# Performance work log

Hardware: AMD Instinct MI355X
Metric: run time of the kernel (lower is better)

The kernel has to match this reference:

```python
import jax, jax.numpy as jnp
import numpy as np

MAX_DEG = 6


def neighbor_lookup(atoms, edges, maskvalue, include_self):
    # atoms: (B, A, F), edges: (B, A, D) with -1 padding
    B, A, F = atoms.shape
    D = edges.shape[-1]
    mask = edges >= 0
    idx = jnp.where(mask, edges, 0).reshape(B, A * D)
    g = jnp.take_along_axis(atoms, idx[:, :, None], axis=1).reshape(B, A, D, F)
    g = jnp.where(mask[..., None], g, maskvalue)
    if include_self:
        g = jnp.concatenate([atoms[:, :, None, :], g], axis=2)  # (B,A,D+1,F)
    return g


def graph_conv(atoms, bonds, edges, W, b):
    # W: (MAX_DEG, F_in+BF, C), b: (MAX_DEG, C)
    deg = (edges >= 0).sum(-1)  # (B, A)
    summed_atoms = neighbor_lookup(atoms, edges, 0.0, True).sum(2)  # self + neighbors
    summed_bonds = bonds.sum(2)
    feats = jnp.concatenate([summed_atoms, summed_bonds], axis=-1)
    out = jnp.zeros(feats.shape[:2] + (W.shape[-1],), feats.dtype)
    for d in range(MAX_DEG):  # small fixed loop over degrees
        h = jax.nn.relu(feats @ W[d] + b[d])
        out = out + jnp.where((deg == d)[..., None], h, 0.0)
    return out


def graph_pool(atoms, edges):
    g = neighbor_lookup(atoms, edges, -jnp.inf, True)  # self included -> finite max
    return g.max(axis=2)


def graph_output(atoms, bonds, edges, Wo, bo):
    deg = (edges >= 0).sum(-1)
    feats = jnp.concatenate([atoms, bonds.sum(2)], axis=-1)
    out = jax.nn.softmax(feats @ Wo + bo, axis=-1)
    mask = (deg != 0)[..., None]  # zero out padded atoms
    return jnp.where(mask, out, 0.0).sum(axis=1)  # (B, hid)


def setup_inputs():
    key = jax.random.key(0)
    ks = jax.random.split(key, 16)
    B, A, D = 4096, 64, 6
    AF, BF, H = 37, 6, 128
    s = lambda k, sh: (jax.random.normal(k, sh, jnp.float32) * 0.05)
    return {
        "atoms": jax.random.normal(ks[0], (B, A, AF), jnp.float32),
        "bonds": jax.random.normal(ks[1], (B, A, D, BF), jnp.float32),
        "edges": jax.random.randint(ks[2], (B, A, D), -1, A),
        "W1": s(ks[3], (MAX_DEG, AF + BF, H)),
        "b1": s(ks[4], (MAX_DEG, H)),
        "W2": s(ks[5], (MAX_DEG, H + BF, H)),
        "b2": s(ks[6], (MAX_DEG, H)),
        "Wo": s(ks[7], (H + BF, H)),
        "bo": s(ks[8], (H,)),
        "Wm1": s(ks[9], (H, H // 2)),
        "bm1": s(ks[10], (H // 2,)),
        "Wm2": s(ks[11], (H // 2, H // 4)),
        "bm2": s(ks[12], (H // 4,)),
        "Wm3": s(ks[13], (H // 4, 1)),
        "bm3": s(ks[14], (1,)),
    }


def reference(atoms, bonds, edges, W1, b1, W2, b2, Wo, bo, Wm1, bm1, Wm2, bm2, Wm3, bm3):
    x = graph_conv(atoms, bonds, edges, W1, b1)
    x = graph_pool(x, edges)
    x = graph_conv(x, bonds, edges, W2, b2)
    x = graph_pool(x, edges)
    fp = graph_output(x, bonds, edges, Wo, bo)
    h = jax.nn.relu(fp @ Wm1 + bm1)
    h = jax.nn.relu(h @ Wm2 + bm2)
    out = (h @ Wm3 + bm3).squeeze()  # (B,)
    return out
```

## Files before the change

### kernel.cpp

```cpp
#include <hip/hip_runtime.h>
#include <math.h>


__device__ __forceinline__ float4 max4(float4 a, float4 b) {
  return make_float4(fmaxf(a.x, b.x), fmaxf(a.y, b.y), fmaxf(a.z, b.z), fmaxf(a.w, b.w));
}

__device__ __forceinline__ float4 nbr_max(const float4* sx4, const int* se, int a, int c4) {
  float4 m = sx4[a * 32 + c4];
#pragma unroll
  for (int d = 0; d < 6; ++d) {
    int e = se[a * 6 + d];
    if (e >= 0) m = max4(m, sx4[e * 32 + c4]);
  }
  return m;
}

__device__ __forceinline__ float4 nbr_sum(const float4* sx4, const int* se, int a, int c4) {
  float4 s = sx4[a * 32 + c4];
#pragma unroll
  for (int d = 0; d < 6; ++d) {
    int e = se[a * 6 + d];
    if (e >= 0) {
      float4 v = sx4[e * 32 + c4];
      s.x += v.x; s.y += v.y; s.z += v.z; s.w += v.w;
    }
  }
  return s;
}

__device__ __forceinline__ float4 nbr_wmax(const float4* sx4, const int* se, const int* sdeg,
                                           int a, int c4) {
  float4 m = make_float4(0.f, 0.f, 0.f, 0.f);
  if (sdeg[a] < 6) m = max4(m, sx4[a * 32 + c4]);
#pragma unroll
  for (int d = 0; d < 6; ++d) {
    int e = se[a * 6 + d];
    if (e >= 0 && sdeg[e] < 6) m = max4(m, sx4[e * 32 + c4]);
  }
  return m;
}

__global__ __launch_bounds__(256, 4) void qsar_fused(
    const float* __restrict__ atoms, const float* __restrict__ bonds,
    const int* __restrict__ edges,
    const float* __restrict__ W1, const float* __restrict__ b1,
    const float* __restrict__ W2, const float* __restrict__ b2,
    const float* __restrict__ Wo, const float* __restrict__ bo,
    const float* __restrict__ Wm1, const float* __restrict__ bm1,
    const float* __restrict__ Wm2, const float* __restrict__ bm2,
    const float* __restrict__ Wm3, const float* __restrict__ bm3,
    float* __restrict__ out)
{
  const int b    = blockIdx.x;
  const int tid  = threadIdx.x;
  const int wid  = tid >> 6;
  const int hid  = tid >> 5;
  const int hl   = tid & 31;

  __shared__ float s_x[64 * 128];
  __shared__ float s_sa[16 * 38];
  __shared__ float s_bsum[64 * 8];
  __shared__ int   s_edges[64 * 6];
  __shared__ int   s_deg[64];
  __shared__ int   s_work[64];
  __shared__ int   s_perm[64];
  __shared__ float s_rsum[64];
  __shared__ int   s_nwork, s_na, s_nz;

  float4* sx4  = reinterpret_cast<float4*>(s_x);
  float*  s_fp = s_sa;
  float*  s_h1 = s_sa + 256;
  float*  s_h2 = s_sa + 320;

  {
    const int* ge = edges + (size_t)b * (64 * 6);
    for (int i = tid; i < 64 * 6; i += 256) s_edges[i] = ge[i];
    const float* gb = bonds + (size_t)b * (64 * 36);
    for (int i = tid; i < 64 * 6; i += 256) {
      int a = i / 6, f = i - a * 6;
      float s = 0.f;
#pragma unroll
      for (int d = 0; d < 6; ++d) s += gb[a * 36 + d * 6 + f];
      s_bsum[a * 8 + f] = s;
    }
#pragma unroll
    for (int j = 0; j < 8; ++j) sx4[tid + j * 256] = make_float4(0.f, 0.f, 0.f, 0.f);
    if (tid == 0) { s_nwork = 0; s_na = 0; s_nz = 0; }
  }
  __syncthreads();

  if (tid < 64) {
    int dcnt = 0;
#pragma unroll
    for (int d = 0; d < 6; ++d) dcnt += (s_edges[tid * 6 + d] >= 0) ? 1 : 0;
    s_deg[tid] = dcnt;
    if (dcnt < 6) { int p = atomicAdd(&s_nwork, 1); s_work[p] = tid; }
  }
  __syncthreads();

  if (tid < 64) {
    int nzf = (s_deg[tid] < 6) ? 1 : 0;
#pragma unroll
    for (int d = 0; d < 6; ++d) {
      int e = s_edges[tid * 6 + d];
      if (e >= 0 && s_deg[e] < 6) nzf = 1;
    }
    if (nzf) { int p = atomicAdd(&s_na, 1); s_perm[p] = tid; }
    else     { int p = atomicAdd(&s_nz, 1); s_perm[63 - p] = tid; }
  }

  {
    const int nw = s_nwork;
    const float* ga = atoms + (size_t)b * (64 * 37);
    const int c0 = hl * 4;
    for (int cb = 0; cb < nw; cb += 16) {
      const int cnt = (nw - cb < 16) ? (nw - cb) : 16;
      for (int i = tid; i < cnt * 37; i += 256) {
        int wi = i / 37, k = i - wi * 37;
        int a = s_work[cb + wi];
        float f = ga[a * 37 + k];
#pragma unroll
        for (int d = 0; d < 6; ++d) {
          int e = s_edges[a * 6 + d];
          if (e >= 0) f += ga[e * 37 + k];
        }
        s_sa[wi * 38 + k] = f;
      }
      __syncthreads();
      for (int w = hid; w < cnt; w += 8) {
        const int a = s_work[cb + w];
        const int d = s_deg[a];
        const float* wp = W1 + d * (43 * 128);
        float4 acc = *reinterpret_cast<const float4*>(&b1[d * 128 + c0]);
#pragma unroll 4
        for (int k = 0; k < 37; ++k) {
          const float f = s_sa[w * 38 + k];
          const float4 w4 = *reinterpret_cast<const float4*>(&wp[k * 128 + c0]);
          acc.x = fmaf(f, w4.x, acc.x); acc.y = fmaf(f, w4.y, acc.y);
          acc.z = fmaf(f, w4.z, acc.z); acc.w = fmaf(f, w4.w, acc.w);
        }
#pragma unroll
        for (int kk = 0; kk < 6; ++kk) {
          const float f = s_bsum[a * 8 + kk];
          const float4 w4 = *reinterpret_cast<const float4*>(&wp[(37 + kk) * 128 + c0]);
          acc.x = fmaf(f, w4.x, acc.x); acc.y = fmaf(f, w4.y, acc.y);
          acc.z = fmaf(f, w4.z, acc.z); acc.w = fmaf(f, w4.w, acc.w);
        }
        *reinterpret_cast<float4*>(&s_x[a * 128 + c0]) =
            make_float4(fmaxf(acc.x, 0.f), fmaxf(acc.y, 0.f),
                        fmaxf(acc.z, 0.f), fmaxf(acc.w, 0.f));
      }
      __syncthreads();
    }
  }
  __syncthreads();

  {
    float4 v0 = nbr_max(sx4, s_edges, (tid + 0 * 256) >> 5, tid & 31);
    float4 v1 = nbr_max(sx4, s_edges, (tid + 1 * 256) >> 5, tid & 31);
    float4 v2 = nbr_max(sx4, s_edges, (tid + 2 * 256) >> 5, tid & 31);
    float4 v3 = nbr_max(sx4, s_edges, (tid + 3 * 256) >> 5, tid & 31);
    float4 v4 = nbr_max(sx4, s_edges, (tid + 4 * 256) >> 5, tid & 31);
    float4 v5 = nbr_max(sx4, s_edges, (tid + 5 * 256) >> 5, tid & 31);
    float4 v6 = nbr_max(sx4, s_edges, (tid + 6 * 256) >> 5, tid & 31);
    float4 v7 = nbr_max(sx4, s_edges, (tid + 7 * 256) >> 5, tid & 31);
    __syncthreads();
    sx4[tid + 0 * 256] = v0; sx4[tid + 1 * 256] = v1;
    sx4[tid + 2 * 256] = v2; sx4[tid + 3 * 256] = v3;
    sx4[tid + 4 * 256] = v4; sx4[tid + 5 * 256] = v5;
    sx4[tid + 6 * 256] = v6; sx4[tid + 7 * 256] = v7;
  }
  __syncthreads();

  {
    const float4 z = make_float4(0.f, 0.f, 0.f, 0.f);
    float4 v0 = z, v1 = z, v2 = z, v3 = z, v4 = z, v5 = z, v6 = z, v7 = z;
    if (s_deg[(tid + 0 * 256) >> 5] < 6) v0 = nbr_sum(sx4, s_edges, (tid + 0 * 256) >> 5, tid & 31);
    if (s_deg[(tid + 1 * 256) >> 5] < 6) v1 = nbr_sum(sx4, s_edges, (tid + 1 * 256) >> 5, tid & 31);
    if (s_deg[(tid + 2 * 256) >> 5] < 6) v2 = nbr_sum(sx4, s_edges, (tid + 2 * 256) >> 5, tid & 31);
    if (s_deg[(tid + 3 * 256) >> 5] < 6) v3 = nbr_sum(sx4, s_edges, (tid + 3 * 256) >> 5, tid & 31);
    if (s_deg[(tid + 4 * 256) >> 5] < 6) v4 = nbr_sum(sx4, s_edges, (tid + 4 * 256) >> 5, tid & 31);
    if (s_deg[(tid + 5 * 256) >> 5] < 6) v5 = nbr_sum(sx4, s_edges, (tid + 5 * 256) >> 5, tid & 31);
    if (s_deg[(tid + 6 * 256) >> 5] < 6) v6 = nbr_sum(sx4, s_edges, (tid + 6 * 256) >> 5, tid & 31);
    if (s_deg[(tid + 7 * 256) >> 5] < 6) v7 = nbr_sum(sx4, s_edges, (tid + 7 * 256) >> 5, tid & 31);
    __syncthreads();
    if (s_deg[(tid + 0 * 256) >> 5] < 6) sx4[tid + 0 * 256] = v0;
    if (s_deg[(tid + 1 * 256) >> 5] < 6) sx4[tid + 1 * 256] = v1;
    if (s_deg[(tid + 2 * 256) >> 5] < 6) sx4[tid + 2 * 256] = v2;
    if (s_deg[(tid + 3 * 256) >> 5] < 6) sx4[tid + 3 * 256] = v3;
    if (s_deg[(tid + 4 * 256) >> 5] < 6) sx4[tid + 4 * 256] = v4;
    if (s_deg[(tid + 5 * 256) >> 5] < 6) sx4[tid + 5 * 256] = v5;
    if (s_deg[(tid + 6 * 256) >> 5] < 6) sx4[tid + 6 * 256] = v6;
    if (s_deg[(tid + 7 * 256) >> 5] < 6) sx4[tid + 7 * 256] = v7;
  }
  __syncthreads();

  {
    const int nw = s_nwork;
    const int c0 = hl * 4;
    for (int w = hid; w < nw; w += 8) {
      const int a = s_work[w];
      const int d = s_deg[a];
      const float* wp = W2 + d * (134 * 128);
      float4 acc = *reinterpret_cast<const float4*>(&b2[d * 128 + c0]);
#pragma unroll 4
      for (int k = 0; k < 128; ++k) {
        const float f = s_x[a * 128 + k];
        const float4 w4 = *reinterpret_cast<const float4*>(&wp[k * 128 + c0]);
        acc.x = fmaf(f, w4.x, acc.x); acc.y = fmaf(f, w4.y, acc.y);
        acc.z = fmaf(f, w4.z, acc.z); acc.w = fmaf(f, w4.w, acc.w);
      }
#pragma unroll
      for (int kk = 0; kk < 6; ++kk) {
        const float f = s_bsum[a * 8 + kk];
        const float4 w4 = *reinterpret_cast<const float4*>(&wp[(128 + kk) * 128 + c0]);
        acc.x = fmaf(f, w4.x, acc.x); acc.y = fmaf(f, w4.y, acc.y);
        acc.z = fmaf(f, w4.z, acc.z); acc.w = fmaf(f, w4.w, acc.w);
      }
      *reinterpret_cast<float4*>(&s_x[a * 128 + c0]) =
          make_float4(fmaxf(acc.x, 0.f), fmaxf(acc.y, 0.f),
                      fmaxf(acc.z, 0.f), fmaxf(acc.w, 0.f));
    }
  }
  __syncthreads();

  {
    float4 v0 = nbr_wmax(sx4, s_edges, s_deg, (tid + 0 * 256) >> 5, tid & 31);
    float4 v1 = nbr_wmax(sx4, s_edges, s_deg, (tid + 1 * 256) >> 5, tid & 31);
    float4 v2 = nbr_wmax(sx4, s_edges, s_deg, (tid + 2 * 256) >> 5, tid & 31);
    float4 v3 = nbr_wmax(sx4, s_edges, s_deg, (tid + 3 * 256) >> 5, tid & 31);
    float4 v4 = nbr_wmax(sx4, s_edges, s_deg, (tid + 4 * 256) >> 5, tid & 31);
    float4 v5 = nbr_wmax(sx4, s_edges, s_deg, (tid + 5 * 256) >> 5, tid & 31);
    float4 v6 = nbr_wmax(sx4, s_edges, s_deg, (tid + 6 * 256) >> 5, tid & 31);
    float4 v7 = nbr_wmax(sx4, s_edges, s_deg, (tid + 7 * 256) >> 5, tid & 31);
    __syncthreads();
    sx4[tid + 0 * 256] = v0; sx4[tid + 1 * 256] = v1;
    sx4[tid + 2 * 256] = v2; sx4[tid + 3 * 256] = v3;
    sx4[tid + 4 * 256] = v4; sx4[tid + 5 * 256] = v5;
    sx4[tid + 6 * 256] = v6; sx4[tid + 7 * 256] = v7;
  }
  __syncthreads();

  {
    const int cg = tid & 31, ag = hid;
    const int c0 = cg * 4;
    const int na = s_na;
    const int nr = (na + 31) >> 5;
    for (int j = 0; j < nr; ++j) {
      const int sl = j * 32 + ag * 4;
      const int at0 = s_perm[sl + 0], at1 = s_perm[sl + 1];
      const int at2 = s_perm[sl + 2], at3 = s_perm[sl + 3];
      float a00 = 0.f, a01 = 0.f, a02 = 0.f, a03 = 0.f;
      float a10 = 0.f, a11 = 0.f, a12 = 0.f, a13 = 0.f;
      float a20 = 0.f, a21 = 0.f, a22 = 0.f, a23 = 0.f;
      float a30 = 0.f, a31 = 0.f, a32 = 0.f, a33 = 0.f;
      if (j * 32 + wid * 8 < na) {
#pragma unroll 4
        for (int k = 0; k < 128; ++k) {
          const float4 w4 = *reinterpret_cast<const float4*>(Wo + k * 128 + c0);
          const float f0 = s_x[at0 * 128 + k], f1 = s_x[at1 * 128 + k];
          const float f2 = s_x[at2 * 128 + k], f3 = s_x[at3 * 128 + k];
          a00 = fmaf(f0, w4.x, a00); a01 = fmaf(f0, w4.y, a01);
          a02 = fmaf(f0, w4.z, a02); a03 = fmaf(f0, w4.w, a03);
          a10 = fmaf(f1, w4.x, a10); a11 = fmaf(f1, w4.y, a11);
          a12 = fmaf(f1, w4.z, a12); a13 = fmaf(f1, w4.w, a13);
          a20 = fmaf(f2, w4.x, a20); a21 = fmaf(f2, w4.y, a21);
          a22 = fmaf(f2, w4.z, a22); a23 = fmaf(f2, w4.w, a23);
          a30 = fmaf(f3, w4.x, a30); a31 = fmaf(f3, w4.y, a31);
          a32 = fmaf(f3, w4.z, a32); a33 = fmaf(f3, w4.w, a33);
        }
#pragma unroll
        for (int kk = 0; kk < 6; ++kk) {
          const float4 w4 = *reinterpret_cast<const float4*>(Wo + (128 + kk) * 128 + c0);
          const float f0 = s_bsum[at0 * 8 + kk], f1 = s_bsum[at1 * 8 + kk];
          const float f2 = s_bsum[at2 * 8 + kk], f3 = s_bsum[at3 * 8 + kk];
          a00 = fmaf(f0, w4.x, a00); a01 = fmaf(f0, w4.y, a01);
          a02 = fmaf(f0, w4.z, a02); a03 = fmaf(f0, w4.w, a03);
          a10 = fmaf(f1, w4.x, a10); a11 = fmaf(f1, w4.y, a11);
          a12 = fmaf(f1, w4.z, a12); a13 = fmaf(f1, w4.w, a13);
          a20 = fmaf(f2, w4.x, a20); a21 = fmaf(f2, w4.y, a21);
          a22 = fmaf(f2, w4.z, a22); a23 = fmaf(f2, w4.w, a23);
          a30 = fmaf(f3, w4.x, a30); a31 = fmaf(f3, w4.y, a31);
          a32 = fmaf(f3, w4.z, a32); a33 = fmaf(f3, w4.w, a33);
        }
      }
      __syncthreads();
      const float4 bo4 = *reinterpret_cast<const float4*>(bo + c0);
      if (sl + 0 < na)
        *reinterpret_cast<float4*>(&s_x[at0 * 128 + c0]) =
            make_float4(a00 + bo4.x, a01 + bo4.y, a02 + bo4.z, a03 + bo4.w);
      if (sl + 1 < na)
        *reinterpret_cast<float4*>(&s_x[at1 * 128 + c0]) =
            make_float4(a10 + bo4.x, a11 + bo4.y, a12 + bo4.z, a13 + bo4.w);
      if (sl + 2 < na)
        *reinterpret_cast<float4*>(&s_x[at2 * 128 + c0]) =
            make_float4(a20 + bo4.x, a21 + bo4.y, a22 + bo4.z, a23 + bo4.w);
      if (sl + 3 < na)
        *reinterpret_cast<float4*>(&s_x[at3 * 128 + c0]) =
            make_float4(a30 + bo4.x, a31 + bo4.y, a32 + bo4.z, a33 + bo4.w);
    }
    const int nz = 64 - na;
    for (int e = tid; e < nz * 128; e += 256) {
      int zi = e >> 7, c = e & 127;
      int a = s_perm[na + zi];
      float acc = bo[c];
#pragma unroll
      for (int kk = 0; kk < 6; ++kk)
        acc = fmaf(s_bsum[a * 8 + kk], Wo[(128 + kk) * 128 + c], acc);
      s_x[a * 128 + c] = acc;
    }
  }
  __syncthreads();

  {
    const int a = tid >> 2, q = tid & 3;
    float* base = &s_x[a * 128 + q * 32];
    const float4 v0 = *reinterpret_cast<const float4*>(base + ((0 + tid) & 7) * 4);
    const float4 v1 = *reinterpret_cast<const float4*>(base + ((1 + tid) & 7) * 4);
    const float4 v2 = *reinterpret_cast<const float4*>(base + ((2 + tid) & 7) * 4);
    const float4 v3 = *reinterpret_cast<const float4*>(base + ((3 + tid) & 7) * 4);
    const float4 v4 = *reinterpret_cast<const float4*>(base + ((4 + tid) & 7) * 4);
    const float4 v5 = *reinterpret_cast<const float4*>(base + ((5 + tid) & 7) * 4);
    const float4 v6 = *reinterpret_cast<const float4*>(base + ((6 + tid) & 7) * 4);
    const float4 v7 = *reinterpret_cast<const float4*>(base + ((7 + tid) & 7) * 4);
    float mx = fmaxf(fmaxf(fmaxf(v0.x, v0.y), fmaxf(v0.z, v0.w)),
                     fmaxf(fmaxf(v1.x, v1.y), fmaxf(v1.z, v1.w)));
    mx = fmaxf(mx, fmaxf(fmaxf(fmaxf(v2.x, v2.y), fmaxf(v2.z, v2.w)),
                         fmaxf(fmaxf(v3.x, v3.y), fmaxf(v3.z, v3.w))));
    mx = fmaxf(mx, fmaxf(fmaxf(fmaxf(v4.x, v4.y), fmaxf(v4.z, v4.w)),
                         fmaxf(fmaxf(v5.x, v5.y), fmaxf(v5.z, v5.w))));
    mx = fmaxf(mx, fmaxf(fmaxf(fmaxf(v6.x, v6.y), fmaxf(v6.z, v6.w)),
                         fmaxf(fmaxf(v7.x, v7.y), fmaxf(v7.z, v7.w))));
    mx = fmaxf(mx, __shfl_xor(mx, 1));
    mx = fmaxf(mx, __shfl_xor(mx, 2));
    float sm = 0.f;
    float4 e0, e1, e2, e3, e4, e5, e6, e7;
    e0.x = __expf(v0.x - mx); e0.y = __expf(v0.y - mx); e0.z = __expf(v0.z - mx); e0.w = __expf(v0.w - mx);
    e1.x = __expf(v1.x - mx); e1.y = __expf(v1.y - mx); e1.z = __expf(v1.z - mx); e1.w = __expf(v1.w - mx);
    e2.x = __expf(v2.x - mx); e2.y = __expf(v2.y - mx); e2.z = __expf(v2.z - mx); e2.w = __expf(v2.w - mx);
    e3.x = __expf(v3.x - mx); e3.y = __expf(v3.y - mx); e3.z = __expf(v3.z - mx); e3.w = __expf(v3.w - mx);
    e4.x = __expf(v4.x - mx); e4.y = __expf(v4.y - mx); e4.z = __expf(v4.z - mx); e4.w = __expf(v4.w - mx);
    e5.x = __expf(v5.x - mx); e5.y = __expf(v5.y - mx); e5.z = __expf(v5.z - mx); e5.w = __expf(v5.w - mx);
    e6.x = __expf(v6.x - mx); e6.y = __expf(v6.y - mx); e6.z = __expf(v6.z - mx); e6.w = __expf(v6.w - mx);
    e7.x = __expf(v7.x - mx); e7.y = __expf(v7.y - mx); e7.z = __expf(v7.z - mx); e7.w = __expf(v7.w - mx);
    sm += e0.x + e0.y + e0.z + e0.w; sm += e1.x + e1.y + e1.z + e1.w;
    sm += e2.x + e2.y + e2.z + e2.w; sm += e3.x + e3.y + e3.z + e3.w;
    sm += e4.x + e4.y + e4.z + e4.w; sm += e5.x + e5.y + e5.z + e5.w;
    sm += e6.x + e6.y + e6.z + e6.w; sm += e7.x + e7.y + e7.z + e7.w;
    *reinterpret_cast<float4*>(base + ((0 + tid) & 7) * 4) = e0;
    *reinterpret_cast<float4*>(base + ((1 + tid) & 7) * 4) = e1;
    *reinterpret_cast<float4*>(base + ((2 + tid) & 7) * 4) = e2;
    *reinterpret_cast<float4*>(base + ((3 + tid) & 7) * 4) = e3;
    *reinterpret_cast<float4*>(base + ((4 + tid) & 7) * 4) = e4;
    *reinterpret_cast<float4*>(base + ((5 + tid) & 7) * 4) = e5;
    *reinterpret_cast<float4*>(base + ((6 + tid) & 7) * 4) = e6;
    *reinterpret_cast<float4*>(base + ((7 + tid) & 7) * 4) = e7;
    sm += __shfl_xor(sm, 1);
    sm += __shfl_xor(sm, 2);
    if (q == 0) s_rsum[a] = (s_deg[a] != 0) ? (1.f / sm) : 0.f;
  }
  __syncthreads();

  {
    const int c = tid & 127, half = tid >> 7;
    float s = 0.f;
    for (int a2 = half * 32; a2 < half * 32 + 32; ++a2)
      s = fmaf(s_x[a2 * 128 + c], s_rsum[a2], s);
    s_fp[half * 128 + c] = s;
  }
  __syncthreads();
  if (tid < 128) s_fp[tid] += s_fp[128 + tid];
  __syncthreads();

  if (tid < 64) {
    float acc = bm1[tid];
    for (int k = 0; k < 128; ++k) acc = fmaf(s_fp[k], Wm1[k * 64 + tid], acc);
    s_h1[tid] = fmaxf(acc, 0.f);
  }
  __syncthreads();
  if (tid < 32) {
    float acc = bm2[tid];
    for (int k = 0; k < 64; ++k) acc = fmaf(s_h1[k], Wm2[k * 32 + tid], acc);
    s_h2[tid] = fmaxf(acc, 0.f);
  }
  __syncthreads();
  if (tid < 64) {
    float p = (tid < 32) ? s_h2[tid] * Wm3[tid] : 0.f;
#pragma unroll
    for (int off = 32; off > 0; off >>= 1) p += __shfl_xor(p, off);
    if (tid == 0) out[b] = p + bm3[0];
  }
}

extern "C" void kernel_launch(void* const* d_in, const int* in_sizes, int n_in,
                              void* d_out, int out_size, void* d_ws, size_t ws_size,
                              hipStream_t stream) {
  const float* atoms = (const float*)d_in[0];
  const float* bonds = (const float*)d_in[1];
  const int*   edges = (const int*)d_in[2];
  const float* W1  = (const float*)d_in[3];
  const float* b1  = (const float*)d_in[4];
  const float* W2  = (const float*)d_in[5];
  const float* b2  = (const float*)d_in[6];
  const float* Wo  = (const float*)d_in[7];
  const float* bo  = (const float*)d_in[8];
  const float* Wm1 = (const float*)d_in[9];
  const float* bm1 = (const float*)d_in[10];
  const float* Wm2 = (const float*)d_in[11];
  const float* bm2 = (const float*)d_in[12];
  const float* Wm3 = (const float*)d_in[13];
  const float* bm3 = (const float*)d_in[14];
  float* out = (float*)d_out;

  const int B = out_size;
  qsar_fused<<<dim3(B), dim3(256), 0, stream>>>(
      atoms, bonds, edges, W1, b1, W2, b2, Wo, bo,
      Wm1, bm1, Wm2, bm2, Wm3, bm3, out);
}
```

Baseline: 245.8 us.

## Stage degree-5 weight tiles in LDS for conv and output matmuls

Weight rows for the most common degree (5) in W1 and W2, and all of Wo, are now loaded cooperatively into a 16-row LDS tile. Each wave reads from that tile instead of issuing its own global float4 loads. The W2 and Wo loops register-prefetch the next tile to overlap global latency. Atoms of other degrees still read global weights directly. This adds about 11 KB of LDS and many extra __syncthreads per tile, and the conv1 chunk size drops from 16 to 8 atoms, which may reduce occupancy or add barrier overhead.

```diff
diff --git a/kernel.cpp b/kernel.cpp
--- a/kernel.cpp
+++ b/kernel.cpp
@@ -54,12 +54,13 @@
 {
   const int b    = blockIdx.x;
   const int tid  = threadIdx.x;
-  const int wid  = tid >> 6;
   const int hid  = tid >> 5;
   const int hl   = tid & 31;
 
   __shared__ float s_x[64 * 128];
-  __shared__ float s_sa[16 * 38];
+  __shared__ float s_wt[16 * 128];
+  __shared__ float s_wtail[6 * 128];
+  __shared__ float s_sa[352];
   __shared__ float s_bsum[64 * 8];
   __shared__ int   s_edges[64 * 6];
   __shared__ int   s_deg[64];
@@ -68,7 +69,9 @@
   __shared__ float s_rsum[64];
   __shared__ int   s_nwork, s_na, s_nz;
 
-  float4* sx4  = reinterpret_cast<float4*>(s_x);
+  float4* sx4      = reinterpret_cast<float4*>(s_x);
+  float4* s_wt4    = reinterpret_cast<float4*>(s_wt);
+  float4* s_wtail4 = reinterpret_cast<float4*>(s_wtail);
   float*  s_fp = s_sa;
   float*  s_h1 = s_sa + 256;
   float*  s_h2 = s_sa + 320;
@@ -113,9 +116,10 @@
   {
     const int nw = s_nwork;
     const float* ga = atoms + (size_t)b * (64 * 37);
+    const float4* W1_5f4 = reinterpret_cast<const float4*>(W1 + 5 * (43 * 128));
     const int c0 = hl * 4;
-    for (int cb = 0; cb < nw; cb += 16) {
-      const int cnt = (nw - cb < 16) ? (nw - cb) : 16;
+    for (int cb = 0; cb < nw; cb += 8) {
+      const int cnt = (nw - cb < 8) ? (nw - cb) : 8;
       for (int i = tid; i < cnt * 37; i += 256) {
         int wi = i / 37, k = i - wi * 37;
         int a = s_work[cb + wi];
@@ -128,30 +132,51 @@
         s_sa[wi * 38 + k] = f;
       }
       __syncthreads();
-      for (int w = hid; w < cnt; w += 8) {
-        const int a = s_work[cb + w];
-        const int d = s_deg[a];
-        const float* wp = W1 + d * (43 * 128);
-        float4 acc = *reinterpret_cast<const float4*>(&b1[d * 128 + c0]);
-#pragma unroll 4
-        for (int k = 0; k < 37; ++k) {
-          const float f = s_sa[w * 38 + k];
-          const float4 w4 = *reinterpret_cast<const float4*>(&wp[k * 128 + c0]);
-          acc.x = fmaf(f, w4.x, acc.x); acc.y = fmaf(f, w4.y, acc.y);
-          acc.z = fmaf(f, w4.z, acc.z); acc.w = fmaf(f, w4.w, acc.w);
-        }
+      const bool have = (hid < cnt);
+      const int a = have ? s_work[cb + hid] : 0;
+      const int d = have ? s_deg[a] : 5;
+      const float4* wdf4 = reinterpret_cast<const float4*>(W1 + d * (43 * 128));
+      float4 acc = *reinterpret_cast<const float4*>(&b1[d * 128 + c0]);
+#pragma unroll
+      for (int t = 0; t < 3; ++t) {
+        const int kt0 = t * 16;
+        const int rows_sa = (t < 2) ? 16 : 5;
+        const int nf4 = rows_sa * 32;
+        const int f2i = tid * 2;
+        if (f2i < nf4)     s_wt4[f2i]     = W1_5f4[kt0 * 32 + f2i];
+        if (f2i + 1 < nf4) s_wt4[f2i + 1] = W1_5f4[kt0 * 32 + f2i + 1];
+        __syncthreads();
+        if (have) {
+          if (d == 5) {
+            for (int k = 0; k < rows_sa; ++k) {
+              const float ff = s_sa[hid * 38 + kt0 + k];
+              const float4 w4 = s_wt4[k * 32 + hl];
+              acc.x = fmaf(ff, w4.x, acc.x); acc.y = fmaf(ff, w4.y, acc.y);
+              acc.z = fmaf(ff, w4.z, acc.z); acc.w = fmaf(ff, w4.w, acc.w);
+            }
+          } else {
+            for (int k = 0; k < rows_sa; ++k) {
+              const float ff = s_sa[hid * 38 + kt0 + k];
+              const float4 w4 = wdf4[(kt0 + k) * 32 + hl];
+              acc.x = fmaf(ff, w4.x, acc.x); acc.y = fmaf(ff, w4.y, acc.y);
+              acc.z = fmaf(ff, w4.z, acc.z); acc.w = fmaf(ff, w4.w, acc.w);
+            }
+          }
+        }
+        __syncthreads();
+      }
+      if (have) {
 #pragma unroll
         for (int kk = 0; kk < 6; ++kk) {
-          const float f = s_bsum[a * 8 + kk];
-          const float4 w4 = *reinterpret_cast<const float4*>(&wp[(37 + kk) * 128 + c0]);
-          acc.x = fmaf(f, w4.x, acc.x); acc.y = fmaf(f, w4.y, acc.y);
-          acc.z = fmaf(f, w4.z, acc.z); acc.w = fmaf(f, w4.w, acc.w);
+          const float ff = s_bsum[a * 8 + kk];
+          const float4 w4 = wdf4[(37 + kk) * 32 + hl];
+          acc.x = fmaf(ff, w4.x, acc.x); acc.y = fmaf(ff, w4.y, acc.y);
+          acc.z = fmaf(ff, w4.z, acc.z); acc.w = fmaf(ff, w4.w, acc.w);
         }
         *reinterpret_cast<float4*>(&s_x[a * 128 + c0]) =
             make_float4(fmaxf(acc.x, 0.f), fmaxf(acc.y, 0.f),
                         fmaxf(acc.z, 0.f), fmaxf(acc.w, 0.f));
       }
-      __syncthreads();
     }
   }
   __syncthreads();
@@ -199,28 +224,53 @@
   {
     const int nw = s_nwork;
     const int c0 = hl * 4;
-    for (int w = hid; w < nw; w += 8) {
-      const int a = s_work[w];
-      const int d = s_deg[a];
-      const float* wp = W2 + d * (134 * 128);
+    const float4* W2_5f4 = reinterpret_cast<const float4*>(W2 + 5 * (134 * 128));
+    for (int g = 0; g < nw; g += 8) {
+      const bool have = (g + hid < nw);
+      const int a = have ? s_work[g + hid] : 0;
+      const int d = have ? s_deg[a] : 5;
+      const float4* wdf4 = reinterpret_cast<const float4*>(W2 + d * (134 * 128));
       float4 acc = *reinterpret_cast<const float4*>(&b2[d * 128 + c0]);
+      float4 p0 = W2_5f4[2 * tid], p1 = W2_5f4[2 * tid + 1];
+      for (int kt = 0; kt < 8; ++kt) {
+        s_wt4[2 * tid] = p0; s_wt4[2 * tid + 1] = p1;
+        __syncthreads();
+        const int ktn = (kt < 7) ? kt + 1 : 7;
+        p0 = W2_5f4[ktn * 512 + 2 * tid]; p1 = W2_5f4[ktn * 512 + 2 * tid + 1];
+        if (have) {
+          const float* xr = &s_x[a * 128 + kt * 16];
+          if (d == 5) {
+#pragma unroll
+            for (int k = 0; k < 16; ++k) {
+              const float ff = xr[k];
+              const float4 w4 = s_wt4[k * 32 + hl];
+              acc.x = fmaf(ff, w4.x, acc.x); acc.y = fmaf(ff, w4.y, acc.y);
+              acc.z = fmaf(ff, w4.z, acc.z); acc.w = fmaf(ff, w4.w, acc.w);
+            }
+          } else {
 #pragma unroll 4
-      for (int k = 0; k < 128; ++k) {
-        const float f = s_x[a * 128 + k];
-        const float4 w4 = *reinterpret_cast<const float4*>(&wp[k * 128 + c0]);
-        acc.x = fmaf(f, w4.x, acc.x); acc.y = fmaf(f, w4.y, acc.y);
-        acc.z = fmaf(f, w4.z, acc.z); acc.w = fmaf(f, w4.w, acc.w);
-      }
-#pragma unroll
-      for (int kk = 0; kk < 6; ++kk) {
-        const float f = s_bsum[a * 8 + kk];
-        const float4 w4 = *reinterpret_cast<const float4*>(&wp[(128 + kk) * 128 + c0]);
-        acc.x = fmaf(f, w4.x, acc.x); acc.y = fmaf(f, w4.y, acc.y);
-        acc.z = fmaf(f, w4.z, acc.z); acc.w = fmaf(f, w4.w, acc.w);
-      }
-      *reinterpret_cast<float4*>(&s_x[a * 128 + c0]) =
-          make_float4(fmaxf(acc.x, 0.f), fmaxf(acc.y, 0.f),
-                      fmaxf(acc.z, 0.f), fmaxf(acc.w, 0.f));
+            for (int k = 0; k < 16; ++k) {
+              const float ff = xr[k];
+              const float4 w4 = wdf4[(kt * 16 + k) * 32 + hl];
+              acc.x = fmaf(ff, w4.x, acc.x); acc.y = fmaf(ff, w4.y, acc.y);
+              acc.z = fmaf(ff, w4.z, acc.z); acc.w = fmaf(ff, w4.w, acc.w);
+            }
+          }
+        }
+        __syncthreads();
+      }
+      if (have) {
+#pragma unroll
+        for (int kk = 0; kk < 6; ++kk) {
+          const float ff = s_bsum[a * 8 + kk];
+          const float4 w4 = wdf4[(128 + kk) * 32 + hl];
+          acc.x = fmaf(ff, w4.x, acc.x); acc.y = fmaf(ff, w4.y, acc.y);
+          acc.z = fmaf(ff, w4.z, acc.z); acc.w = fmaf(ff, w4.w, acc.w);
+        }
+        *reinterpret_cast<float4*>(&s_x[a * 128 + c0]) =
+            make_float4(fmaxf(acc.x, 0.f), fmaxf(acc.y, 0.f),
+                        fmaxf(acc.z, 0.f), fmaxf(acc.w, 0.f));
+      }
     }
   }
   __syncthreads();
@@ -243,36 +293,50 @@
   __syncthreads();
 
   {
-    const int cg = tid & 31, ag = hid;
+    const int cg = hl;
     const int c0 = cg * 4;
     const int na = s_na;
     const int nr = (na + 31) >> 5;
+    const float4* Wof4 = reinterpret_cast<const float4*>(Wo);
+    for (int i = tid; i < 768; i += 256) s_wtail[i] = Wo[128 * 128 + i];
     for (int j = 0; j < nr; ++j) {
-      const int sl = j * 32 + ag * 4;
+      const int sl = j * 32 + hid * 4;
+      const bool act = (sl < na);
       const int at0 = s_perm[sl + 0], at1 = s_perm[sl + 1];
       const int at2 = s_perm[sl + 2], at3 = s_perm[sl + 3];
       float a00 = 0.f, a01 = 0.f, a02 = 0.f, a03 = 0.f;
       float a10 = 0.f, a11 = 0.f, a12 = 0.f, a13 = 0.f;
       float a20 = 0.f, a21 = 0.f, a22 = 0.f, a23 = 0.f;
       float a30 = 0.f, a31 = 0.f, a32 = 0.f, a33 = 0.f;
-      if (j * 32 + wid * 8 < na) {
-#pragma unroll 4
-        for (int k = 0; k < 128; ++k) {
-          const float4 w4 = *reinterpret_cast<const float4*>(Wo + k * 128 + c0);
-          const float f0 = s_x[at0 * 128 + k], f1 = s_x[at1 * 128 + k];
-          const float f2 = s_x[at2 * 128 + k], f3 = s_x[at3 * 128 + k];
-          a00 = fmaf(f0, w4.x, a00); a01 = fmaf(f0, w4.y, a01);
-          a02 = fmaf(f0, w4.z, a02); a03 = fmaf(f0, w4.w, a03);
-          a10 = fmaf(f1, w4.x, a10); a11 = fmaf(f1, w4.y, a11);
-          a12 = fmaf(f1, w4.z, a12); a13 = fmaf(f1, w4.w, a13);
-          a20 = fmaf(f2, w4.x, a20); a21 = fmaf(f2, w4.y, a21);
-          a22 = fmaf(f2, w4.z, a22); a23 = fmaf(f2, w4.w, a23);
-          a30 = fmaf(f3, w4.x, a30); a31 = fmaf(f3, w4.y, a31);
-          a32 = fmaf(f3, w4.z, a32); a33 = fmaf(f3, w4.w, a33);
-        }
+      float4 p0 = Wof4[2 * tid], p1 = Wof4[2 * tid + 1];
+      for (int kt = 0; kt < 8; ++kt) {
+        s_wt4[2 * tid] = p0; s_wt4[2 * tid + 1] = p1;
+        __syncthreads();
+        const int ktn = (kt < 7) ? kt + 1 : 7;
+        p0 = Wof4[ktn * 512 + 2 * tid]; p1 = Wof4[ktn * 512 + 2 * tid + 1];
+        if (act) {
+#pragma unroll
+          for (int k = 0; k < 16; ++k) {
+            const float4 w4 = s_wt4[k * 32 + cg];
+            const int kb = kt * 16 + k;
+            const float f0 = s_x[at0 * 128 + kb], f1 = s_x[at1 * 128 + kb];
+            const float f2 = s_x[at2 * 128 + kb], f3 = s_x[at3 * 128 + kb];
+            a00 = fmaf(f0, w4.x, a00); a01 = fmaf(f0, w4.y, a01);
+            a02 = fmaf(f0, w4.z, a02); a03 = fmaf(f0, w4.w, a03);
+            a10 = fmaf(f1, w4.x, a10); a11 = fmaf(f1, w4.y, a11);
+            a12 = fmaf(f1, w4.z, a12); a13 = fmaf(f1, w4.w, a13);
+            a20 = fmaf(f2, w4.x, a20); a21 = fmaf(f2, w4.y, a21);
+            a22 = fmaf(f2, w4.z, a22); a23 = fmaf(f2, w4.w, a23);
+            a30 = fmaf(f3, w4.x, a30); a31 = fmaf(f3, w4.y, a31);
+            a32 = fmaf(f3, w4.z, a32); a33 = fmaf(f3, w4.w, a33);
+          }
+        }
+        __syncthreads();
+      }
+      if (act) {
 #pragma unroll
         for (int kk = 0; kk < 6; ++kk) {
-          const float4 w4 = *reinterpret_cast<const float4*>(Wo + (128 + kk) * 128 + c0);
+          const float4 w4 = s_wtail4[kk * 32 + cg];
           const float f0 = s_bsum[at0 * 8 + kk], f1 = s_bsum[at1 * 8 + kk];
           const float f2 = s_bsum[at2 * 8 + kk], f3 = s_bsum[at3 * 8 + kk];
           a00 = fmaf(f0, w4.x, a00); a01 = fmaf(f0, w4.y, a01);
@@ -285,7 +349,6 @@
           a32 = fmaf(f3, w4.z, a32); a33 = fmaf(f3, w4.w, a33);
         }
       }
-      __syncthreads();
       const float4 bo4 = *reinterpret_cast<const float4*>(bo + c0);
       if (sl + 0 < na)
         *reinterpret_cast<float4*>(&s_x[at0 * 128 + c0]) =
@@ -300,6 +363,7 @@
         *reinterpret_cast<float4*>(&s_x[at3 * 128 + c0]) =
             make_float4(a30 + bo4.x, a31 + bo4.y, a32 + bo4.z, a33 + bo4.w);
     }
+    __syncthreads();
     const int nz = 64 - na;
     for (int e = tid; e < nz * 128; e += 256) {
       int zi = e >> 7, c = e & 127;
@@ -307,7 +371,7 @@
       float acc = bo[c];
 #pragma unroll
       for (int kk = 0; kk < 6; ++kk)
-        acc = fmaf(s_bsum[a * 8 + kk], Wo[(128 + kk) * 128 + c], acc);
+        acc = fmaf(s_bsum[a * 8 + kk], s_wtail[kk * 128 + c], acc);
       s_x[a * 128 + c] = acc;
     }
   }
```

After: 363.7 us. +48.0%, slower.
